# Optimization experiments

Hardware: AMD Instinct MI355X
Metric: run time of the kernel (lower is better)

The kernel has to match this reference:

```python
import jax, jax.numpy as jnp
import numpy as np

N_NODES = 100000

def gcn_conv(x, W, b, src, dst, n):
    # PyG GCNConv: add self-loops, symmetric normalization, scatter-add aggregation.
    xw = x @ W  # [N, out]
    loop = jnp.arange(n, dtype=src.dtype)
    s = jnp.concatenate([src, loop])
    d = jnp.concatenate([dst, loop])
    deg = jax.ops.segment_sum(jnp.ones_like(d, dtype=xw.dtype), d, num_segments=n)
    inv_sqrt = jnp.where(deg > 0, jax.lax.rsqrt(jnp.maximum(deg, 1.0)), 0.0)
    norm = inv_sqrt[s] * inv_sqrt[d]  # [E+N]
    msg = xw[s] * norm[:, None]       # gather + scale
    out = jax.ops.segment_sum(msg, d, num_segments=n)  # scatter-add
    return out + b

def setup_inputs() -> dict:
    key = jax.random.key(0)
    k = jax.random.split(key, 6)
    x = jax.random.normal(k[0], (N_NODES, 128), dtype=jnp.float32)
    edge_index = jax.random.randint(k[1], (2, 3200000), 0, N_NODES, dtype=jnp.int64 if jax.config.jax_enable_x64 else jnp.int32)
    edge_label_index = jax.random.randint(k[2], (2, 200000), 0, N_NODES, dtype=edge_index.dtype)
    W1 = jax.random.normal(k[3], (128, 32), dtype=jnp.float32) * (1.0 / np.sqrt(128))
    b1 = jnp.zeros((32,), dtype=jnp.float32)
    W2 = jax.random.normal(k[4], (32, 16), dtype=jnp.float32) * (1.0 / np.sqrt(32))
    b2 = jnp.zeros((16,), dtype=jnp.float32)
    return {"x": x, "edge_index": edge_index, "edge_label_index": edge_label_index,
            "W1": W1, "b1": b1, "W2": W2, "b2": b2}

def reference(x, edge_index, edge_label_index, W1, b1, W2, b2):
    src, dst = edge_index[0], edge_index[1]
    n = x.shape[0]
    # encode (eval mode: dropout is identity)
    h = gcn_conv(x, W1, b1, src, dst, n)
    h = jax.nn.relu(h)
    z = gcn_conv(h, W2, b2, src, dst, n)
    # decode: dot product over candidate edges
    logits = jnp.sum(z[edge_label_index[0]] * z[edge_label_index[1]], axis=-1)
    return logits
```

## Files before the change

### kernel.cpp

```cpp
#include <hip/hip_runtime.h>
#include <hip/hip_fp16.h>


#define NPB 128
#define NBMAX 1024
#define A3_CHUNK 8192

__global__ __launch_bounds__(256) void k_a1(const int* __restrict__ dst,
                                            int* __restrict__ bcnt, int E, int NB) {
    __shared__ int lb[NBMAX];
    int t = threadIdx.x;
    for (int i = t; i < NB; i += 256) lb[i] = 0;
    __syncthreads();
    for (int e = blockIdx.x * 256 + t; e < E; e += gridDim.x * 256)
        atomicAdd(&lb[dst[e] >> 7], 1);
    __syncthreads();
    for (int i = t; i < NB; i += 256) {
        int c = lb[i];
        if (c) atomicAdd(&bcnt[i], c);
    }
}

__global__ __launch_bounds__(256) void k_scanb(const int* __restrict__ bcnt,
                                               int* __restrict__ bbase,
                                               int* __restrict__ bcursor, int NB) {
    __shared__ int sh[256];
    int t = threadIdx.x;
    int i0 = t * 4;
    int v0 = (i0 + 0 < NB) ? bcnt[i0 + 0] : 0;
    int v1 = (i0 + 1 < NB) ? bcnt[i0 + 1] : 0;
    int v2 = (i0 + 2 < NB) ? bcnt[i0 + 2] : 0;
    int v3 = (i0 + 3 < NB) ? bcnt[i0 + 3] : 0;
    sh[t] = v0 + v1 + v2 + v3;
    __syncthreads();
    for (int off = 1; off < 256; off <<= 1) {
        int add = (t >= off) ? sh[t - off] : 0;
        __syncthreads();
        sh[t] += add;
        __syncthreads();
    }
    int run = (t > 0) ? sh[t - 1] : 0;
    if (i0 + 0 < NB) { bbase[i0 + 0] = run; bcursor[i0 + 0] = run; } run += v0;
    if (i0 + 1 < NB) { bbase[i0 + 1] = run; bcursor[i0 + 1] = run; } run += v1;
    if (i0 + 2 < NB) { bbase[i0 + 2] = run; bcursor[i0 + 2] = run; } run += v2;
    if (i0 + 3 < NB) { bbase[i0 + 3] = run; bcursor[i0 + 3] = run; }
    if (t == 255) bbase[NB] = sh[255];
}

__global__ __launch_bounds__(256) void k_a3(const int* __restrict__ src,
                                            const int* __restrict__ dst,
                                            int* __restrict__ bcursor,
                                            unsigned* __restrict__ eb, int E, int NB) {
    __shared__ int lhist[NBMAX];
    __shared__ int lbase[NBMAX];
    int t = threadIdx.x;
    int e0 = blockIdx.x * A3_CHUNK;
    for (int i = t; i < NB; i += 256) lhist[i] = 0;
    __syncthreads();
    unsigned myp[32];
    int myb[32];
#pragma unroll
    for (int j = 0; j < 32; ++j) {
        int e = e0 + j * 256 + t;
        if (e < E) {
            int s = src[e], d = dst[e];
            myb[j] = d >> 7;
            myp[j] = ((unsigned)s << 7) | (unsigned)(d & 127);
            atomicAdd(&lhist[myb[j]], 1);
        } else {
            myb[j] = -1;
        }
    }
    __syncthreads();
    for (int i = t; i < NB; i += 256) {
        int c = lhist[i];
        lbase[i] = c ? atomicAdd(&bcursor[i], c) : 0;
        lhist[i] = 0;
    }
    __syncthreads();
#pragma unroll
    for (int j = 0; j < 32; ++j) {
        if (myb[j] >= 0) {
            int r = atomicAdd(&lhist[myb[j]], 1);
            eb[lbase[myb[j]] + r] = myp[j];
        }
    }
}

__global__ __launch_bounds__(256) void k_csr(const int* __restrict__ bbase,
                                             const unsigned* __restrict__ eb,
                                             int* __restrict__ col,
                                             int* __restrict__ rp,
                                             float* __restrict__ inv,
                                             int n, int E, int NB) {
    __shared__ int cnt[4][NPB];
    __shared__ int cur[4][NPB];
    __shared__ int tot[NPB];
    int t = threadIdx.x, b = blockIdx.x;
    int wv = t >> 6;
    int nbase = b * NPB;
    int beg = bbase[b], end = bbase[b + 1];
    for (int i = t; i < 4 * NPB; i += 256) ((int*)cnt)[i] = 0;
    __syncthreads();
    for (int i = beg + t; i < end; i += 256) atomicAdd(&cnt[wv][eb[i] & 127u], 1);
    __syncthreads();
    int c = 0;
    if (t < NPB) {
        c = cnt[0][t] + cnt[1][t] + cnt[2][t] + cnt[3][t];
        tot[t] = c;
    }
    __syncthreads();
    for (int off = 1; off < NPB; off <<= 1) {
        int v = (t < NPB && t >= off) ? tot[t - off] : 0;
        __syncthreads();
        if (t < NPB) tot[t] += v;
        __syncthreads();
    }
    if (t < NPB) {
        int excl = tot[t] - c;
        int run = beg + excl;
#pragma unroll
        for (int r = 0; r < 4; ++r) { cur[r][t] = run; run += cnt[r][t]; }
        int node = nbase + t;
        if (node < n) {
            rp[node] = beg + excl;
            inv[node] = rsqrtf((float)(c + 1));
        }
    }
    if (b == NB - 1 && t == 0) rp[n] = E;
    __syncthreads();
    for (int i = beg + t; i < end; i += 256) {
        unsigned p = eb[i];
        int pos = atomicAdd(&cur[wv][p & 127u], 1);
        col[pos] = (int)(p >> 7);
    }
}

__global__ __launch_bounds__(256) void k_xw(const float* __restrict__ x,
                                            const float* __restrict__ W1,
                                            const float* __restrict__ inv,
                                            uint2* __restrict__ X, int n) {
    __shared__ float xsh[128 * 128];
    __shared__ float W1s[128 * 32];
    int t = threadIdx.x;
    int base = blockIdx.x * 128;
#pragma unroll
    for (int i = 0; i < 16; ++i) W1s[i * 256 + t] = W1[i * 256 + t];
    {
        int nl = t >> 1, kh = (t & 1) * 64;
        int node = base + nl;
        if (node < n) {
            const float4* xr = (const float4*)(x + (size_t)node * 128 + kh);
#pragma unroll
            for (int kk = 0; kk < 16; ++kk) {
                float4 v = xr[kk];
                int k = kh + kk * 4;
                xsh[(k + 0) * 128 + nl] = v.x;
                xsh[(k + 1) * 128 + nl] = v.y;
                xsh[(k + 2) * 128 + nl] = v.z;
                xsh[(k + 3) * 128 + nl] = v.w;
            }
        } else {
#pragma unroll
            for (int kk = 0; kk < 64; ++kk) xsh[(kh + kk) * 128 + nl] = 0.0f;
        }
    }
    __syncthreads();
    int tc = t & 7, tr = t >> 3;
    float acc[4][4] = {};
#pragma unroll 8
    for (int k = 0; k < 128; ++k) {
        float4 xv = *(const float4*)&xsh[k * 128 + 4 * tr];
        float4 wv = *(const float4*)&W1s[k * 32 + 4 * tc];
        acc[0][0] += xv.x * wv.x; acc[0][1] += xv.x * wv.y; acc[0][2] += xv.x * wv.z; acc[0][3] += xv.x * wv.w;
        acc[1][0] += xv.y * wv.x; acc[1][1] += xv.y * wv.y; acc[1][2] += xv.y * wv.z; acc[1][3] += xv.y * wv.w;
        acc[2][0] += xv.z * wv.x; acc[2][1] += xv.z * wv.y; acc[2][2] += xv.z * wv.z; acc[2][3] += xv.z * wv.w;
        acc[3][0] += xv.w * wv.x; acc[3][1] += xv.w * wv.y; acc[3][2] += xv.w * wv.z; acc[3][3] += xv.w * wv.w;
    }
#pragma unroll
    for (int i = 0; i < 4; ++i) {
        int node = base + 4 * tr + i;
        if (node < n) {
            float iw = inv[node];
            __half2 p0 = __floats2half2_rn(acc[i][0] * iw, acc[i][1] * iw);
            __half2 p1 = __floats2half2_rn(acc[i][2] * iw, acc[i][3] * iw);
            uint2 u;
            u.x = *(unsigned*)&p0;
            u.y = *(unsigned*)&p1;
            X[(size_t)node * 8 + tc] = u;
        }
    }
}

__device__ __forceinline__ void add8(float* a, uint4 v) {
    union { uint4 u; __half h[8]; } cv;
    cv.u = v;
#pragma unroll
    for (int j = 0; j < 8; ++j) a[j] = fmaf(__half2float(cv.h[j]), 1.0f, a[j]);
}

__device__ __forceinline__ void add4(float* a, uint2 v) {
    union { uint2 u; __half h[4]; } cv;
    cv.u = v;
#pragma unroll
    for (int j = 0; j < 4; ++j) a[j] = fmaf(__half2float(cv.h[j]), 1.0f, a[j]);
}

__global__ __launch_bounds__(256) void k_agg1(const int* __restrict__ rp,
                                              const int* __restrict__ col,
                                              const uint4* __restrict__ X4,
                                              const float* __restrict__ inv,
                                              const float* __restrict__ b1,
                                              const float* __restrict__ W2,
                                              __half* __restrict__ hws, int n) {
    int wid = (blockIdx.x * 256 + threadIdx.x) >> 6;
    int nw = (gridDim.x * 256) >> 6;
    int lane = threadIdx.x & 63;
    int q = lane & 3, g = lane >> 2;
    int c = lane & 15, r = lane >> 4;
    float w2r[8], bb[8];
#pragma unroll
    for (int j = 0; j < 8; ++j) w2r[j] = W2[(8 * r + j) * 16 + c];
#pragma unroll
    for (int j = 0; j < 8; ++j) bb[j] = b1[8 * q + j];
    for (int w = wid; w < n; w += nw) {
        int beg = rp[w], end = rp[w + 1];
        float a0[8] = {}, a1[8] = {};
        if (g == 0) add8(a0, X4[(size_t)w * 4 + q]);
        int i = beg + g;
        for (; i + 16 < end; i += 32) {
            int s0 = col[i], s1 = col[i + 16];
            uint4 v0 = X4[(size_t)s0 * 4 + q];
            uint4 v1 = X4[(size_t)s1 * 4 + q];
            add8(a0, v0);
            add8(a1, v1);
        }
        for (; i < end; i += 16) add8(a0, X4[(size_t)col[i] * 4 + q]);
#pragma unroll
        for (int j = 0; j < 8; ++j) a0[j] += a1[j];
#pragma unroll
        for (int m = 4; m < 64; m <<= 1)
#pragma unroll
            for (int j = 0; j < 8; ++j) a0[j] += __shfl_xor(a0[j], m);
        float iw = inv[w];
        float h[8];
#pragma unroll
        for (int j = 0; j < 8; ++j) h[j] = fmaxf(iw * a0[j] + bb[j], 0.0f);
        float s = 0.0f;
#pragma unroll
        for (int j = 0; j < 8; ++j) s += __shfl(h[j], r) * w2r[j];
        s += __shfl_xor(s, 16);
        s += __shfl_xor(s, 32);
        if (lane < 16) hws[(size_t)w * 16 + c] = __float2half(s * iw);
    }
}

__global__ __launch_bounds__(256) void k_agg2(const int* __restrict__ rp,
                                              const int* __restrict__ col,
                                              const uint2* __restrict__ H2,
                                              const float* __restrict__ inv,
                                              const float* __restrict__ b2,
                                              uint2* __restrict__ z, int n) {
    int wid = (blockIdx.x * 256 + threadIdx.x) >> 6;
    int nw = (gridDim.x * 256) >> 6;
    int lane = threadIdx.x & 63;
    int q = lane & 3, g = lane >> 2;
    float bb[4];
#pragma unroll
    for (int j = 0; j < 4; ++j) bb[j] = b2[4 * q + j];
    for (int w = wid; w < n; w += nw) {
        int beg = rp[w], end = rp[w + 1];
        float a0[4] = {}, a1[4] = {};
        if (g == 0) add4(a0, H2[(size_t)w * 4 + q]);
        int i = beg + g;
        for (; i + 16 < end; i += 32) {
            int s0 = col[i], s1 = col[i + 16];
            uint2 v0 = H2[(size_t)s0 * 4 + q];
            uint2 v1 = H2[(size_t)s1 * 4 + q];
            add4(a0, v0);
            add4(a1, v1);
        }
        for (; i < end; i += 16) add4(a0, H2[(size_t)col[i] * 4 + q]);
#pragma unroll
        for (int j = 0; j < 4; ++j) a0[j] += a1[j];
#pragma unroll
        for (int m = 4; m < 64; m <<= 1)
#pragma unroll
            for (int j = 0; j < 4; ++j) a0[j] += __shfl_xor(a0[j], m);
        float iw = inv[w];
        if (lane < 4) {
            __half2 p0 = __floats2half2_rn(iw * a0[0] + bb[0], iw * a0[1] + bb[1]);
            __half2 p1 = __floats2half2_rn(iw * a0[2] + bb[2], iw * a0[3] + bb[3]);
            uint2 u;
            u.x = *(unsigned*)&p0;
            u.y = *(unsigned*)&p1;
            z[(size_t)w * 4 + q] = u;
        }
    }
}

__device__ __forceinline__ float dot8h(uint4 u, uint4 v, float s) {
    const __half2* pu = (const __half2*)&u;
    const __half2* pv = (const __half2*)&v;
#pragma unroll
    for (int i = 0; i < 4; ++i) {
#if __has_builtin(__builtin_amdgcn_fdot2)
        s = __builtin_amdgcn_fdot2(pu[i], pv[i], s, false);
#else
        float2 a = __half22float2(pu[i]);
        float2 b = __half22float2(pv[i]);
        s += a.x * b.x + a.y * b.y;
#endif
    }
    return s;
}

__global__ void k_decode(const int* __restrict__ eli, const uint4* __restrict__ z4,
                         float* __restrict__ out, int L) {
    int e = blockIdx.x * blockDim.x + threadIdx.x;
    if (e >= L) return;
    int a = eli[e], b = eli[L + e];
    uint4 ua0 = z4[(size_t)a * 2], ua1 = z4[(size_t)a * 2 + 1];
    uint4 ub0 = z4[(size_t)b * 2], ub1 = z4[(size_t)b * 2 + 1];
    out[e] = dot8h(ua1, ub1, dot8h(ua0, ub0, 0.0f));
}

extern "C" void kernel_launch(void* const* d_in, const int* in_sizes, int n_in,
                              void* d_out, int out_size, void* d_ws, size_t ws_size,
                              hipStream_t stream) {
    const float* x   = (const float*)d_in[0];
    const int*   ei  = (const int*)d_in[1];
    const int*   eli = (const int*)d_in[2];
    const float* W1  = (const float*)d_in[3];
    const float* b1  = (const float*)d_in[4];
    const float* W2  = (const float*)d_in[5];
    const float* b2  = (const float*)d_in[6];
    float* out = (float*)d_out;

    int n = in_sizes[0] / 128;
    int E = in_sizes[1] / 2;
    int L = in_sizes[2] / 2;
    const int* src = ei;
    const int* dst = ei + E;
    int NB = (n + NPB - 1) / NPB;

    uint2* X   = (uint2*)d_ws;
    uint2* hws = X + (size_t)n * 8;
    uint2* z   = hws + (size_t)n * 4;
    float* inv = (float*)(z + (size_t)n * 4);
    int* rp      = (int*)(inv + n);
    unsigned* eb = (unsigned*)(rp + n + 1);
    int* col     = (int*)(eb + E);
    int* bcnt    = col + E;
    int* bbase   = bcnt + NB;
    int* bcursor = bbase + NB + 1;

    hipMemsetAsync(bcnt, 0, NB * sizeof(int), stream);
    k_a1<<<512, 256, 0, stream>>>(dst, bcnt, E, NB);
    k_scanb<<<1, 256, 0, stream>>>(bcnt, bbase, bcursor, NB);
    k_a3<<<(E + A3_CHUNK - 1) / A3_CHUNK, 256, 0, stream>>>(src, dst, bcursor, eb, E, NB);
    k_csr<<<NB, 256, 0, stream>>>(bbase, eb, col, rp, inv, n, E, NB);
    k_xw<<<(n + 127) / 128, 256, 0, stream>>>(x, W1, inv, X, n);
    k_agg1<<<2048, 256, 0, stream>>>(rp, col, (const uint4*)X, inv, b1, W2, (__half*)hws, n);
    k_agg2<<<2048, 256, 0, stream>>>(rp, col, hws, inv, b2, z, n);
    k_decode<<<(L + 255) / 256, 256, 0, stream>>>(eli, (const uint4*)z, out, L);
}
```

Before: 315.4 us.

## Pad CSR rows to multiples of four and aggregate with 8 threads per node

The CSR build now pads each node's neighbor list to a multiple of four. Padding entries point at an extra zero row appended to the feature buffers, so the aggregation kernels can read column indices as aligned int4 loads with no tail loop. Both aggregation kernels move from one 64-lane wave per node (strided edges plus a cross-lane shuffle reduction) to 8 threads per node, each owning a slice of the feature vector. Each thread keeps four independent gathers in flight and no reduction across the edge dimension is needed. This costs a second scan, some extra col storage and wasted gathers on padding entries, and agg1 now stages W2 in shared memory.

```diff
diff --git a/kernel.cpp b/kernel.cpp
--- a/kernel.cpp
+++ b/kernel.cpp
@@ -23,15 +23,18 @@
 
 __global__ __launch_bounds__(256) void k_scanb(const int* __restrict__ bcnt,
                                                int* __restrict__ bbase,
-                                               int* __restrict__ bcursor, int NB) {
+                                               int* __restrict__ bcursor,
+                                               int* __restrict__ pbase, int NB) {
     __shared__ int sh[256];
     int t = threadIdx.x;
     int i0 = t * 4;
-    int v0 = (i0 + 0 < NB) ? bcnt[i0 + 0] : 0;
-    int v1 = (i0 + 1 < NB) ? bcnt[i0 + 1] : 0;
-    int v2 = (i0 + 2 < NB) ? bcnt[i0 + 2] : 0;
-    int v3 = (i0 + 3 < NB) ? bcnt[i0 + 3] : 0;
-    sh[t] = v0 + v1 + v2 + v3;
+    int v[4], p[4];
+#pragma unroll
+    for (int j = 0; j < 4; ++j) {
+        v[j] = (i0 + j < NB) ? bcnt[i0 + j] : 0;
+        p[j] = ((v[j] + 3) & ~3) + 384;
+    }
+    sh[t] = v[0] + v[1] + v[2] + v[3];
     __syncthreads();
     for (int off = 1; off < 256; off <<= 1) {
         int add = (t >= off) ? sh[t - off] : 0;
@@ -40,11 +43,28 @@
         __syncthreads();
     }
     int run = (t > 0) ? sh[t - 1] : 0;
-    if (i0 + 0 < NB) { bbase[i0 + 0] = run; bcursor[i0 + 0] = run; } run += v0;
-    if (i0 + 1 < NB) { bbase[i0 + 1] = run; bcursor[i0 + 1] = run; } run += v1;
-    if (i0 + 2 < NB) { bbase[i0 + 2] = run; bcursor[i0 + 2] = run; } run += v2;
-    if (i0 + 3 < NB) { bbase[i0 + 3] = run; bcursor[i0 + 3] = run; }
-    if (t == 255) bbase[NB] = sh[255];
+    int total = sh[255];
+#pragma unroll
+    for (int j = 0; j < 4; ++j) {
+        if (i0 + j < NB) { bbase[i0 + j] = run; bcursor[i0 + j] = run; }
+        run += v[j];
+    }
+    if (t == 255) bbase[NB] = total;
+    __syncthreads();
+    sh[t] = p[0] + p[1] + p[2] + p[3];
+    __syncthreads();
+    for (int off = 1; off < 256; off <<= 1) {
+        int add = (t >= off) ? sh[t - off] : 0;
+        __syncthreads();
+        sh[t] += add;
+        __syncthreads();
+    }
+    int run2 = (t > 0) ? sh[t - 1] : 0;
+#pragma unroll
+    for (int j = 0; j < 4; ++j) {
+        if (i0 + j < NB) pbase[i0 + j] = run2;
+        run2 += p[j];
+    }
 }
 
 __global__ __launch_bounds__(256) void k_a3(const int* __restrict__ src,
@@ -88,11 +108,13 @@
 }
 
 __global__ __launch_bounds__(256) void k_csr(const int* __restrict__ bbase,
+                                             const int* __restrict__ pbase,
                                              const unsigned* __restrict__ eb,
                                              int* __restrict__ col,
-                                             int* __restrict__ rp,
+                                             int* __restrict__ rpbeg,
+                                             int* __restrict__ rpcnt,
                                              float* __restrict__ inv,
-                                             int n, int E, int NB) {
+                                             int n, int NB) {
     __shared__ int cnt[4][NPB];
     __shared__ int cur[4][NPB];
     __shared__ int tot[NPB];
@@ -100,14 +122,16 @@
     int wv = t >> 6;
     int nbase = b * NPB;
     int beg = bbase[b], end = bbase[b + 1];
+    int pb = pbase[b];
     for (int i = t; i < 4 * NPB; i += 256) ((int*)cnt)[i] = 0;
     __syncthreads();
     for (int i = beg + t; i < end; i += 256) atomicAdd(&cnt[wv][eb[i] & 127u], 1);
     __syncthreads();
-    int c = 0;
+    int c = 0, pc = 0;
     if (t < NPB) {
         c = cnt[0][t] + cnt[1][t] + cnt[2][t] + cnt[3][t];
-        tot[t] = c;
+        pc = (c + 3) & ~3;
+        tot[t] = pc;
     }
     __syncthreads();
     for (int off = 1; off < NPB; off <<= 1) {
@@ -117,17 +141,18 @@
         __syncthreads();
     }
     if (t < NPB) {
-        int excl = tot[t] - c;
-        int run = beg + excl;
+        int base_t = pb + (tot[t] - pc);
+        int run = base_t;
 #pragma unroll
         for (int r = 0; r < 4; ++r) { cur[r][t] = run; run += cnt[r][t]; }
         int node = nbase + t;
         if (node < n) {
-            rp[node] = beg + excl;
+            rpbeg[node] = base_t;
+            rpcnt[node] = pc;
             inv[node] = rsqrtf((float)(c + 1));
-        }
-    }
-    if (b == NB - 1 && t == 0) rp[n] = E;
+            for (int j = c; j < pc; ++j) col[base_t + j] = n;
+        }
+    }
     __syncthreads();
     for (int i = beg + t; i < end; i += 256) {
         unsigned p = eb[i];
@@ -139,7 +164,8 @@
 __global__ __launch_bounds__(256) void k_xw(const float* __restrict__ x,
                                             const float* __restrict__ W1,
                                             const float* __restrict__ inv,
-                                            uint2* __restrict__ X, int n) {
+                                            uint2* __restrict__ X,
+                                            unsigned* __restrict__ hws0, int n) {
     __shared__ float xsh[128 * 128];
     __shared__ float W1s[128 * 32];
     int t = threadIdx.x;
@@ -164,6 +190,10 @@
 #pragma unroll
             for (int kk = 0; kk < 64; ++kk) xsh[(kh + kk) * 128 + nl] = 0.0f;
         }
+    }
+    if (blockIdx.x == 0) {
+        if (t < 8) X[(size_t)n * 8 + t] = make_uint2(0u, 0u);
+        else if (t < 16) hws0[(size_t)n * 8 + (t - 8)] = 0u;
     }
     __syncthreads();
     int tc = t & 7, tr = t >> 3;
@@ -192,111 +222,101 @@
     }
 }
 
-__device__ __forceinline__ void add8(float* a, uint4 v) {
-    union { uint4 u; __half h[8]; } cv;
-    cv.u = v;
-#pragma unroll
-    for (int j = 0; j < 8; ++j) a[j] = fmaf(__half2float(cv.h[j]), 1.0f, a[j]);
-}
-
-__device__ __forceinline__ void add4(float* a, uint2 v) {
+__device__ __forceinline__ void add4h(float* a, uint2 v) {
     union { uint2 u; __half h[4]; } cv;
     cv.u = v;
 #pragma unroll
     for (int j = 0; j < 4; ++j) a[j] = fmaf(__half2float(cv.h[j]), 1.0f, a[j]);
 }
 
-__global__ __launch_bounds__(256) void k_agg1(const int* __restrict__ rp,
+__device__ __forceinline__ void add2h(float* a, unsigned v) {
+    union { unsigned u; __half h[2]; } cv;
+    cv.u = v;
+    a[0] = fmaf(__half2float(cv.h[0]), 1.0f, a[0]);
+    a[1] = fmaf(__half2float(cv.h[1]), 1.0f, a[1]);
+}
+
+__global__ __launch_bounds__(256) void k_agg1(const int* __restrict__ rpbeg,
+                                              const int* __restrict__ rpcnt,
                                               const int* __restrict__ col,
-                                              const uint4* __restrict__ X4,
+                                              const uint2* __restrict__ X2,
                                               const float* __restrict__ inv,
                                               const float* __restrict__ b1,
                                               const float* __restrict__ W2,
-                                              __half* __restrict__ hws, int n) {
-    int wid = (blockIdx.x * 256 + threadIdx.x) >> 6;
-    int nw = (gridDim.x * 256) >> 6;
-    int lane = threadIdx.x & 63;
-    int q = lane & 3, g = lane >> 2;
-    int c = lane & 15, r = lane >> 4;
-    float w2r[8], bb[8];
-#pragma unroll
-    for (int j = 0; j < 8; ++j) w2r[j] = W2[(8 * r + j) * 16 + c];
-#pragma unroll
-    for (int j = 0; j < 8; ++j) bb[j] = b1[8 * q + j];
-    for (int w = wid; w < n; w += nw) {
-        int beg = rp[w], end = rp[w + 1];
-        float a0[8] = {}, a1[8] = {};
-        if (g == 0) add8(a0, X4[(size_t)w * 4 + q]);
-        int i = beg + g;
-        for (; i + 16 < end; i += 32) {
-            int s0 = col[i], s1 = col[i + 16];
-            uint4 v0 = X4[(size_t)s0 * 4 + q];
-            uint4 v1 = X4[(size_t)s1 * 4 + q];
-            add8(a0, v0);
-            add8(a1, v1);
-        }
-        for (; i < end; i += 16) add8(a0, X4[(size_t)col[i] * 4 + q]);
-#pragma unroll
-        for (int j = 0; j < 8; ++j) a0[j] += a1[j];
-#pragma unroll
-        for (int m = 4; m < 64; m <<= 1)
-#pragma unroll
-            for (int j = 0; j < 8; ++j) a0[j] += __shfl_xor(a0[j], m);
-        float iw = inv[w];
-        float h[8];
-#pragma unroll
-        for (int j = 0; j < 8; ++j) h[j] = fmaxf(iw * a0[j] + bb[j], 0.0f);
-        float s = 0.0f;
-#pragma unroll
-        for (int j = 0; j < 8; ++j) s += __shfl(h[j], r) * w2r[j];
-        s += __shfl_xor(s, 16);
-        s += __shfl_xor(s, 32);
-        if (lane < 16) hws[(size_t)w * 16 + c] = __float2half(s * iw);
-    }
-}
-
-__global__ __launch_bounds__(256) void k_agg2(const int* __restrict__ rp,
+                                              __half2* __restrict__ hws, int n) {
+    __shared__ float W2s[512];
+    int t = threadIdx.x;
+    W2s[t] = W2[t];
+    W2s[256 + t] = W2[256 + t];
+    __syncthreads();
+    int w = (blockIdx.x * 256 + t) >> 3;
+    if (w >= n) return;
+    int q = t & 7;
+    int grpbase = (t & 63) & 56;
+    float bb[4];
+#pragma unroll
+    for (int j = 0; j < 4; ++j) bb[j] = b1[4 * q + j];
+    int beg = rpbeg[w], endp = beg + rpcnt[w];
+    float a[4] = {};
+    add4h(a, X2[(size_t)w * 8 + q]);
+    for (int i = beg; i < endp; i += 4) {
+        int4 c4 = *(const int4*)(col + i);
+        uint2 v0 = X2[(size_t)c4.x * 8 + q];
+        uint2 v1 = X2[(size_t)c4.y * 8 + q];
+        uint2 v2 = X2[(size_t)c4.z * 8 + q];
+        uint2 v3 = X2[(size_t)c4.w * 8 + q];
+        add4h(a, v0);
+        add4h(a, v1);
+        add4h(a, v2);
+        add4h(a, v3);
+    }
+    float iw = inv[w];
+    float h[4];
+#pragma unroll
+    for (int j = 0; j < 4; ++j) h[j] = fmaxf(iw * a[j] + bb[j], 0.0f);
+    float s0 = 0.0f, s1 = 0.0f;
+#pragma unroll
+    for (int qq = 0; qq < 8; ++qq) {
+#pragma unroll
+        for (int j = 0; j < 4; ++j) {
+            float hv = __shfl(h[j], grpbase + qq);
+            float2 wv = *(const float2*)&W2s[(4 * qq + j) * 16 + 2 * q];
+            s0 = fmaf(hv, wv.x, s0);
+            s1 = fmaf(hv, wv.y, s1);
+        }
+    }
+    hws[(size_t)w * 8 + q] = __floats2half2_rn(s0 * iw, s1 * iw);
+}
+
+__global__ __launch_bounds__(256) void k_agg2(const int* __restrict__ rpbeg,
+                                              const int* __restrict__ rpcnt,
                                               const int* __restrict__ col,
-                                              const uint2* __restrict__ H2,
+                                              const unsigned* __restrict__ H,
                                               const float* __restrict__ inv,
                                               const float* __restrict__ b2,
-                                              uint2* __restrict__ z, int n) {
-    int wid = (blockIdx.x * 256 + threadIdx.x) >> 6;
-    int nw = (gridDim.x * 256) >> 6;
-    int lane = threadIdx.x & 63;
-    int q = lane & 3, g = lane >> 2;
-    float bb[4];
-#pragma unroll
-    for (int j = 0; j < 4; ++j) bb[j] = b2[4 * q + j];
-    for (int w = wid; w < n; w += nw) {
-        int beg = rp[w], end = rp[w + 1];
-        float a0[4] = {}, a1[4] = {};
-        if (g == 0) add4(a0, H2[(size_t)w * 4 + q]);
-        int i = beg + g;
-        for (; i + 16 < end; i += 32) {
-            int s0 = col[i], s1 = col[i + 16];
-            uint2 v0 = H2[(size_t)s0 * 4 + q];
-            uint2 v1 = H2[(size_t)s1 * 4 + q];
-            add4(a0, v0);
-            add4(a1, v1);
-        }
-        for (; i < end; i += 16) add4(a0, H2[(size_t)col[i] * 4 + q]);
-#pragma unroll
-        for (int j = 0; j < 4; ++j) a0[j] += a1[j];
-#pragma unroll
-        for (int m = 4; m < 64; m <<= 1)
-#pragma unroll
-            for (int j = 0; j < 4; ++j) a0[j] += __shfl_xor(a0[j], m);
-        float iw = inv[w];
-        if (lane < 4) {
-            __half2 p0 = __floats2half2_rn(iw * a0[0] + bb[0], iw * a0[1] + bb[1]);
-            __half2 p1 = __floats2half2_rn(iw * a0[2] + bb[2], iw * a0[3] + bb[3]);
-            uint2 u;
-            u.x = *(unsigned*)&p0;
-            u.y = *(unsigned*)&p1;
-            z[(size_t)w * 4 + q] = u;
-        }
-    }
+                                              unsigned* __restrict__ z, int n) {
+    int t = threadIdx.x;
+    int w = (blockIdx.x * 256 + t) >> 3;
+    if (w >= n) return;
+    int q = t & 7;
+    float bb0 = b2[2 * q], bb1 = b2[2 * q + 1];
+    int beg = rpbeg[w], endp = beg + rpcnt[w];
+    float a[2] = {};
+    add2h(a, H[(size_t)w * 8 + q]);
+    for (int i = beg; i < endp; i += 4) {
+        int4 c4 = *(const int4*)(col + i);
+        unsigned v0 = H[(size_t)c4.x * 8 + q];
+        unsigned v1 = H[(size_t)c4.y * 8 + q];
+        unsigned v2 = H[(size_t)c4.z * 8 + q];
+        unsigned v3 = H[(size_t)c4.w * 8 + q];
+        add2h(a, v0);
+        add2h(a, v1);
+        add2h(a, v2);
+        add2h(a, v3);
+    }
+    float iw = inv[w];
+    __half2 r = __floats2half2_rn(iw * a[0] + bb0, iw * a[1] + bb1);
+    z[(size_t)w * 8 + q] = *(unsigned*)&r;
 }
 
 __device__ __forceinline__ float dot8h(uint4 u, uint4 v, float s) {
@@ -344,24 +364,26 @@
     const int* dst = ei + E;
     int NB = (n + NPB - 1) / NPB;
 
-    uint2* X   = (uint2*)d_ws;
-    uint2* hws = X + (size_t)n * 8;
-    uint2* z   = hws + (size_t)n * 4;
-    float* inv = (float*)(z + (size_t)n * 4);
-    int* rp      = (int*)(inv + n);
-    unsigned* eb = (unsigned*)(rp + n + 1);
-    int* col     = (int*)(eb + E);
-    int* bcnt    = col + E;
-    int* bbase   = bcnt + NB;
-    int* bcursor = bbase + NB + 1;
+    uint2* X       = (uint2*)d_ws;
+    unsigned* hws  = (unsigned*)(X + (size_t)(n + 1) * 8);
+    unsigned* z    = hws + (size_t)(n + 1) * 8;
+    float* inv     = (float*)(z + (size_t)n * 8);
+    int* rpbeg     = (int*)(inv + n);
+    int* rpcnt     = rpbeg + n;
+    unsigned* eb   = (unsigned*)(rpcnt + n);
+    int* col       = (int*)(eb + E);
+    int* bcnt      = col + E + 400 * NB;
+    int* bbase     = bcnt + NB;
+    int* pbase     = bbase + NB + 1;
+    int* bcursor   = pbase + NB + 1;
 
     hipMemsetAsync(bcnt, 0, NB * sizeof(int), stream);
     k_a1<<<512, 256, 0, stream>>>(dst, bcnt, E, NB);
-    k_scanb<<<1, 256, 0, stream>>>(bcnt, bbase, bcursor, NB);
+    k_scanb<<<1, 256, 0, stream>>>(bcnt, bbase, bcursor, pbase, NB);
     k_a3<<<(E + A3_CHUNK - 1) / A3_CHUNK, 256, 0, stream>>>(src, dst, bcursor, eb, E, NB);
-    k_csr<<<NB, 256, 0, stream>>>(bbase, eb, col, rp, inv, n, E, NB);
-    k_xw<<<(n + 127) / 128, 256, 0, stream>>>(x, W1, inv, X, n);
-    k_agg1<<<2048, 256, 0, stream>>>(rp, col, (const uint4*)X, inv, b1, W2, (__half*)hws, n);
-    k_agg2<<<2048, 256, 0, stream>>>(rp, col, hws, inv, b2, z, n);
+    k_csr<<<NB, 256, 0, stream>>>(bbase, pbase, eb, col, rpbeg, rpcnt, inv, n, NB);
+    k_xw<<<(n + 127) / 128, 256, 0, stream>>>(x, W1, inv, X, hws, n);
+    k_agg1<<<((size_t)n * 8 + 255) / 256, 256, 0, stream>>>(rpbeg, rpcnt, col, X, inv, b1, W2, (__half2*)hws, n);
+    k_agg2<<<((size_t)n * 8 + 255) / 256, 256, 0, stream>>>(rpbeg, rpcnt, col, hws, inv, b2, z, n);
     k_decode<<<(L + 255) / 256, 256, 0, stream>>>(eli, (const uint4*)z, out, L);
 }
```

New measurement: 279.6 us. 1.13x faster.
